# Performance work log

Hardware: AMD Instinct MI355X
Metric: run time of the kernel (lower is better)

## Reference

```python
import jax, jax.numpy as jnp
import numpy as np

B, W, F, H = 2048, 128, 8, 256
LN_EPS = 1e-5


def _gru_cell(h, xt, Wih, Whh, bih, bhh):
    # PyTorch GRU cell. Wih: [3H, Fin], Whh: [3H, H]
    gi = xt @ Wih.T + bih            # [B, 3H]
    gh = h @ Whh.T + bhh             # [B, 3H]
    ir, iz, inn = jnp.split(gi, 3, axis=-1)
    hr, hz, hn = jnp.split(gh, 3, axis=-1)
    r = jax.nn.sigmoid(ir + hr)
    z = jax.nn.sigmoid(iz + hz)
    n = jnp.tanh(inn + r * hn)
    return (1.0 - z) * n + z * h


def setup_inputs() -> dict:
    key = jax.random.key(0)
    ks = jax.random.split(key, 12)
    s = 1.0 / np.sqrt(H)   # torch GRU init: U(-1/sqrt(H), 1/sqrt(H))
    sp = 1.0 / np.sqrt(2 * H)  # torch Linear init fan_in = 2H
    u = lambda k, shp, sc: jax.random.uniform(k, shp, jnp.float32, -sc, sc)
    return {
        "x": jax.random.normal(ks[0], (B, W, F), jnp.float32),
        "Wih_f": u(ks[1], (3 * H, F), s), "Whh_f": u(ks[2], (3 * H, H), s),
        "bih_f": u(ks[3], (3 * H,), s), "bhh_f": u(ks[4], (3 * H,), s),
        "Wih_b": u(ks[5], (3 * H, F), s), "Whh_b": u(ks[6], (3 * H, H), s),
        "bih_b": u(ks[7], (3 * H,), s), "bhh_b": u(ks[8], (3 * H,), s),
        "Wp": u(ks[9], (H, 2 * H), sp), "bp": u(ks[10], (H,), sp),
        "gamma": jnp.ones((H,), jnp.float32), "beta": jnp.zeros((H,), jnp.float32),
    }


def reference(x, Wih_f, Whh_f, bih_f, bhh_f, Wih_b, Whh_b, bih_b, bhh_b, Wp, bp, gamma, beta):
    b = x.shape[0]
    h0 = jnp.zeros((b, H), x.dtype)
    xs = jnp.swapaxes(x, 0, 1)  # [W, B, F]
    # Forward direction: only the final hidden state is used (out[:, -1, :H]).
    h_fwd, _ = jax.lax.scan(
        lambda h, xt: (_gru_cell(h, xt, Wih_f, Whh_f, bih_f, bhh_f), None), h0, xs)
    # Backward direction output at the LAST time index is its FIRST step
    # (reversed scan starting from h0 on x[:, -1]).
    h_bwd = _gru_cell(h0, x[:, -1, :], Wih_b, Whh_b, bih_b, bhh_b)
    last = jnp.concatenate([h_fwd, h_bwd], axis=-1)  # [B, 2H]
    y = jax.nn.gelu(last @ Wp.T + bp, approximate=False)
    mu = jnp.mean(y, axis=-1, keepdims=True)
    var = jnp.var(y, axis=-1, keepdims=True)
    yn = (y - mu) * jax.lax.rsqrt(var + LN_EPS)
    return yn * gamma + beta  # dropout is identity in eval mode
```

## Files before the change

### kernel.cpp

```cpp
#include <hip/hip_runtime.h>
#include <hip/hip_bf16.h>

#define BDIM 2048
#define WDIM 128
#define FDIM 8
#define HDIM 256

typedef __bf16 b8 __attribute__((ext_vector_type(8)));
typedef __bf16 b4 __attribute__((ext_vector_type(4)));
typedef float f32x4 __attribute__((ext_vector_type(4)));
typedef long l64;

#define L2E  1.44269504088896f
#define L2E2 2.88539008177793f

#define OFF_RZ8 0
#define OFF_NB  131072
#define OFF_WI8 262144
#define OFF_WIN 278528
#define OFF_WP  294912
#define OFF_XB  557056

#define MFMA(a,b,c)  __builtin_amdgcn_mfma_f32_16x16x32_bf16((a),(b),(c),0,0,0)
#define MFMA8(a,b,c) __builtin_amdgcn_mfma_f32_16x16x32_fp8_fp8((a),(b),(c),0,0,0)

static __device__ __forceinline__ float sig_(float v) {
    return __builtin_amdgcn_rcpf(1.0f + __expf(-v));
}
static __device__ __forceinline__ float tanh_(float v) {
    return fmaf(-2.0f, __builtin_amdgcn_rcpf(1.0f + __expf(2.0f * v)), 1.0f);
}

static __device__ __forceinline__ l64 pk8(const float* v) {
    int lo = __builtin_amdgcn_cvt_pk_fp8_f32(v[0], v[1], 0, false);
    lo = __builtin_amdgcn_cvt_pk_fp8_f32(v[2], v[3], lo, true);
    int hi = __builtin_amdgcn_cvt_pk_fp8_f32(v[4], v[5], 0, false);
    hi = __builtin_amdgcn_cvt_pk_fp8_f32(v[6], v[7], hi, true);
    return ((l64)(unsigned)hi << 32) | (unsigned)lo;
}
static __device__ __forceinline__ l64 b8_to_f8(b8 v) {
    float f[8];
    #pragma unroll
    for (int e = 0; e < 8; ++e) f[e] = (float)v[e];
    return pk8(f);
}

__global__ void pack_kernel(const float* __restrict__ x,
                            const float* __restrict__ Wih_f,
                            const float* __restrict__ Whh_f,
                            const float* __restrict__ bih_f,
                            const float* __restrict__ bhh_f,
                            const float* __restrict__ Wp,
                            unsigned char* __restrict__ ws)
{
    int idx = blockIdx.x * 256 + threadIdx.x;
    if (idx < 16384) {
        int l = idx & 63, f = idx >> 6;
        int kt = f & 7, nt = (f >> 3) & 1, g = (f >> 4) & 1, w = f >> 5;
        int gch = g * HDIM + 32 * w + 16 * nt + (l & 15);
        int kb = kt * 32 + (l >> 4) * 8;
        float v[8];
        #pragma unroll
        for (int e = 0; e < 8; ++e) v[e] = -L2E * Whh_f[gch * HDIM + kb + e];
        ((l64*)(ws + OFF_RZ8))[idx] = pk8(v);
    } else if (idx < 24576) {
        int j = idx - 16384;
        int l = j & 63, f = j >> 6;
        int kt = f & 7, nt = (f >> 3) & 1, w = f >> 4;
        int gch = 2 * HDIM + 32 * w + 16 * nt + (l & 15);
        int kb = kt * 32 + (l >> 4) * 8;
        b8 v;
        #pragma unroll
        for (int e = 0; e < 8; ++e) v[e] = (__bf16)(L2E2 * Whh_f[gch * HDIM + kb + e]);
        ((b8*)(ws + OFF_NB))[j] = v;
    } else if (idx < 26624) {
        int j = idx - 24576;
        int l = j & 63, f = j >> 6;
        int nt = f & 1, g = (f >> 1) & 1, w = f >> 2;
        int gch = g * HDIM + 32 * w + 16 * nt + (l & 15);
        int lq = l >> 4;
        float v[8];
        #pragma unroll
        for (int e = 0; e < 8; ++e) v[e] = 0.0f;
        if (lq == 0) {
            #pragma unroll
            for (int e = 0; e < 8; ++e) v[e] = -L2E * Wih_f[gch * FDIM + e];
        } else if (lq == 1) {
            v[0] = -L2E * (bih_f[gch] + bhh_f[gch]);
        }
        ((l64*)(ws + OFF_WI8))[j] = pk8(v);
    } else if (idx < 27648) {
        int j = idx - 26624;
        int l = j & 63, f = j >> 6;
        int nt = f & 1, w = f >> 1;
        int gch = 2 * HDIM + 32 * w + 16 * nt + (l & 15);
        int lq = l >> 4;
        b8 v;
        #pragma unroll
        for (int e = 0; e < 8; ++e) v[e] = (__bf16)0.0f;
        if (lq == 0) {
            #pragma unroll
            for (int e = 0; e < 8; ++e) v[e] = (__bf16)(L2E2 * Wih_f[gch * FDIM + e]);
        } else if (lq == 1) {
            v[0] = (__bf16)(L2E2 * bih_f[gch]);
        }
        ((b8*)(ws + OFF_WIN))[j] = v;
    } else if (idx < 44032) {
        int j = idx - 27648;
        int l = j & 63, nk = j >> 6;
        int NT = nk >> 4, kt = nk & 15;
        int col = NT * 16 + (l & 15);
        int kb = kt * 32 + (l >> 4) * 8;
        b8 v;
        #pragma unroll
        for (int e = 0; e < 8; ++e) v[e] = (__bf16)Wp[col * (2 * HDIM) + kb + e];
        ((b8*)(ws + OFF_WP))[j] = v;
    } else if (idx < 44032 + 262144) {
        int j = idx - 44032;
        const float* src = x + j * 8;
        b8 v;
        #pragma unroll
        for (int e = 0; e < 8; ++e) v[e] = (__bf16)src[e];
        ((b8*)(ws + OFF_XB))[j] = v;
    }
}

__global__ __launch_bounds__(512, 2)
void gru_main_kernel(const float* __restrict__ x,
                     const float* __restrict__ bhh_f,
                     const float* __restrict__ Wih_b, const float* __restrict__ bih_b,
                     const float* __restrict__ bhh_b,
                     const float* __restrict__ bp,
                     const float* __restrict__ gamma, const float* __restrict__ beta,
                     const unsigned char* __restrict__ ws,
                     float* __restrict__ out)
{
    __shared__ __align__(16) unsigned char smem[32768];
    __bf16* hbB = (__bf16*)smem;
    unsigned char* hb8 = smem + 16384;
    __bf16 (*lastb)[2 * HDIM] = (__bf16(*)[2 * HDIM])smem;
    float  (*ybuf)[HDIM]      = (float(*)[HDIM])(smem + 16384);

    const int tid = threadIdx.x, lane = tid & 63, w = tid >> 6;
    const int l15 = lane & 15, lq = lane >> 4;
    const int blockRow = blockIdx.x * 16;

    const l64* wsRZ8 = (const l64*)(ws + OFF_RZ8);
    const b8*  wsNB  = (const b8*)(ws + OFF_NB);
    const l64* wsWI8 = (const l64*)(ws + OFF_WI8);
    const b8*  wsWIN = (const b8*)(ws + OFF_WIN);
    const b8*  wsWP  = (const b8*)(ws + OFF_WP);
    const b8*  xB    = (const b8*)(ws + OFF_XB);

    const f32x4 zero4 = {0.f, 0.f, 0.f, 0.f};

    *(f32x4*)(smem + tid * 16) = zero4;
    *(f32x4*)(smem + 8192 + tid * 16) = zero4;
    *(f32x4*)(smem + 16384 + tid * 16) = zero4;

    l64 whr8[2][8], whz8[2][8], wir8[2], wiz8[2];
    b8 wnnB[2][8], winB[2];
    #pragma unroll
    for (int nt = 0; nt < 2; ++nt) {
        #pragma unroll
        for (int kt = 0; kt < 8; ++kt) {
            whr8[nt][kt] = wsRZ8[((w * 4 + 0 + nt) * 8 + kt) * 64 + lane];
            whz8[nt][kt] = wsRZ8[((w * 4 + 2 + nt) * 8 + kt) * 64 + lane];
            wnnB[nt][kt] = wsNB[((w * 2 + nt) * 8 + kt) * 64 + lane];
        }
        wir8[nt] = wsWI8[(w * 4 + 0 + nt) * 64 + lane];
        wiz8[nt] = wsWI8[(w * 4 + 2 + nt) * 64 + lane];
        winB[nt] = wsWIN[(w * 2 + nt) * 64 + lane];
    }
    #pragma unroll
    for (int nt = 0; nt < 2; ++nt) {
        #pragma unroll
        for (int kt = 0; kt < 8; ++kt) {
            asm volatile("" : "+v"(whr8[nt][kt]));
            asm volatile("" : "+v"(whz8[nt][kt]));
            asm volatile("" : "+a"(wnnB[nt][kt]));
        }
        asm volatile("" : "+v"(wir8[nt]));
        asm volatile("" : "+v"(wiz8[nt]));
        asm volatile("" : "+v"(winB[nt]));
    }

    float4 t0v = *(const float4*)&bhh_f[2 * HDIM + 32 * w + 0  + 4 * lq];
    float4 t1v = *(const float4*)&bhh_f[2 * HDIM + 32 * w + 16 + 4 * lq];
    f32x4 bnv0, bnv1;
    bnv0[0] = L2E2 * t0v.x; bnv0[1] = L2E2 * t0v.y; bnv0[2] = L2E2 * t0v.z; bnv0[3] = L2E2 * t0v.w;
    bnv1[0] = L2E2 * t1v.x; bnv1[1] = L2E2 * t1v.y; bnv1[2] = L2E2 * t1v.z; bnv1[3] = L2E2 * t1v.w;

    b8 xc;
    #pragma unroll
    for (int e = 0; e < 8; ++e) xc[e] = (__bf16)0.0f;
    if (lq == 1) xc[0] = (__bf16)1.0f;

    f32x4 h0 = zero4, h1 = zero4;

    const int kswz = (8 * lq) ^ ((l15 & 7) << 3);
    const int wswz = (l15 & 7) << 3;
    const b8* xRow = xB + (blockRow + l15) * WDIM;

    b8 xf = xc;
    if (lane < 16) xf = xRow[0];

    __syncthreads();

    int cur = 0;
    for (int t = 0; t < WDIM; ++t) {
        b8 xn = xc;
        if (lane < 16) xn = xRow[(t + 1) & 127];

        l64 xf8 = b8_to_f8(xf);

        f32x4 aR0 = MFMA8(wir8[0], xf8, zero4);
        f32x4 aR1 = MFMA8(wir8[1], xf8, zero4);
        f32x4 aZ0 = MFMA8(wiz8[0], xf8, zero4);
        f32x4 aZ1 = MFMA8(wiz8[1], xf8, zero4);
        f32x4 aNX0 = MFMA(winB[0], xf, zero4);
        f32x4 aNX1 = MFMA(winB[1], xf, zero4);
        f32x4 aNH0 = bnv0, aNH1 = bnv1;

        const __bf16* hcB = hbB + cur * 4096 + l15 * 256;
        const unsigned char* hc8 = hb8 + cur * 4096 + l15 * 256;
        #pragma unroll
        for (int kt = 0; kt < 8; ++kt) {
            b8 hfB  = *(const b8*)(hcB + ((kt << 5) ^ kswz));
            l64 hf8 = *(const l64*)(hc8 + ((kt << 5) ^ kswz));
            aR0  = MFMA8(whr8[0][kt], hf8, aR0);
            aR1  = MFMA8(whr8[1][kt], hf8, aR1);
            aZ0  = MFMA8(whz8[0][kt], hf8, aZ0);
            aZ1  = MFMA8(whz8[1][kt], hf8, aZ1);
            aNH0 = MFMA(wnnB[0][kt], hfB, aNH0);
            aNH1 = MFMA(wnnB[1][kt], hfB, aNH1);
        }

        __bf16* hnB = hbB + (cur ^ 1) * 4096;
        unsigned char* hn8 = hb8 + (cur ^ 1) * 4096 + l15 * 256;
        b4 v0, v1;
        float hv0[4], hv1[4];
        #pragma unroll
        for (int j = 0; j < 4; ++j) {
            float r = __builtin_amdgcn_rcpf(1.0f + __builtin_amdgcn_exp2f(aR0[j]));
            float z = __builtin_amdgcn_rcpf(1.0f + __builtin_amdgcn_exp2f(aZ0[j]));
            float u = fmaf(r, aNH0[j], aNX0[j]);
            float n = fmaf(-2.0f, __builtin_amdgcn_rcpf(1.0f + __builtin_amdgcn_exp2f(u)), 1.0f);
            float hv = n + z * (h0[j] - n);
            h0[j] = hv; v0[j] = (__bf16)hv; hv0[j] = hv;

            r = __builtin_amdgcn_rcpf(1.0f + __builtin_amdgcn_exp2f(aR1[j]));
            z = __builtin_amdgcn_rcpf(1.0f + __builtin_amdgcn_exp2f(aZ1[j]));
            u = fmaf(r, aNH1[j], aNX1[j]);
            n = fmaf(-2.0f, __builtin_amdgcn_rcpf(1.0f + __builtin_amdgcn_exp2f(u)), 1.0f);
            hv = n + z * (h1[j] - n);
            h1[j] = hv; v1[j] = (__bf16)hv; hv1[j] = hv;
        }
        *(b4*)(hnB + l15 * 256 + ((32 * w + 0  + 4 * lq) ^ wswz)) = v0;
        *(b4*)(hnB + l15 * 256 + ((32 * w + 16 + 4 * lq) ^ wswz)) = v1;
        int p0 = __builtin_amdgcn_cvt_pk_fp8_f32(hv0[0], hv0[1], 0, false);
        p0 = __builtin_amdgcn_cvt_pk_fp8_f32(hv0[2], hv0[3], p0, true);
        int p1 = __builtin_amdgcn_cvt_pk_fp8_f32(hv1[0], hv1[1], 0, false);
        p1 = __builtin_amdgcn_cvt_pk_fp8_f32(hv1[2], hv1[3], p1, true);
        *(int*)(hn8 + ((32 * w + 0  + 4 * lq) ^ wswz)) = p0;
        *(int*)(hn8 + ((32 * w + 16 + 4 * lq) ^ wswz)) = p1;

        xf = xn;
        cur ^= 1;
        __syncthreads();
    }

    {
        b4 v0, v1;
        #pragma unroll
        for (int j = 0; j < 4; ++j) { v0[j] = (__bf16)h0[j]; v1[j] = (__bf16)h1[j]; }
        *(b4*)(&lastb[l15][0] + ((32 * w + 0  + 4 * lq) ^ wswz)) = v0;
        *(b4*)(&lastb[l15][0] + ((32 * w + 16 + 4 * lq) ^ wswz)) = v1;
    }

    {
        const int trow = tid >> 5;
        const int cb = tid & 31;
        const float4* xr = (const float4*)(x + (blockRow + trow) * WDIM * FDIM + 127 * FDIM);
        float4 xv0 = xr[0], xv1 = xr[1];
        const float4* wb = (const float4*)Wih_b;
        #pragma unroll
        for (int jj = 0; jj < 8; ++jj) {
            int ch = cb + 32 * jj;
            float4 a0 = wb[ch * 2],               a1 = wb[ch * 2 + 1];
            float4 b0 = wb[(HDIM + ch) * 2],      b1 = wb[(HDIM + ch) * 2 + 1];
            float4 c0v = wb[(2 * HDIM + ch) * 2], c1 = wb[(2 * HDIM + ch) * 2 + 1];
            float ir = bih_b[ch]
                + xv0.x * a0.x + xv0.y * a0.y + xv0.z * a0.z + xv0.w * a0.w
                + xv1.x * a1.x + xv1.y * a1.y + xv1.z * a1.z + xv1.w * a1.w;
            float iz = bih_b[HDIM + ch]
                + xv0.x * b0.x + xv0.y * b0.y + xv0.z * b0.z + xv0.w * b0.w
                + xv1.x * b1.x + xv1.y * b1.y + xv1.z * b1.z + xv1.w * b1.w;
            float inn = bih_b[2 * HDIM + ch]
                + xv0.x * c0v.x + xv0.y * c0v.y + xv0.z * c0v.z + xv0.w * c0v.w
                + xv1.x * c1.x + xv1.y * c1.y + xv1.z * c1.z + xv1.w * c1.w;
            float r = sig_(ir + bhh_b[ch]);
            float z = sig_(iz + bhh_b[HDIM + ch]);
            float n = tanh_(fmaf(r, bhh_b[2 * HDIM + ch], inn));
            float hbw = (1.0f - z) * n;
            int c2 = HDIM + ch;
            lastb[trow][c2 ^ ((trow & 7) << 3)] = (__bf16)hbw;
        }
    }
    __syncthreads();

    {
        f32x4 pacc[2];
        #pragma unroll
        for (int nt = 0; nt < 2; ++nt) {
            int col = 32 * w + nt * 16 + l15;
            float b = bp[col];
            pacc[nt][0] = b; pacc[nt][1] = b; pacc[nt][2] = b; pacc[nt][3] = b;
        }
        #pragma unroll
        for (int kt = 0; kt < 16; ++kt) {
            int c = (kt * 32 + lq * 8) ^ ((l15 & 7) << 3);
            b8 a = *(const b8*)&lastb[l15][c];
            #pragma unroll
            for (int nt = 0; nt < 2; ++nt)
                pacc[nt] = MFMA(a, wsWP[((2 * w + nt) * 16 + kt) * 64 + lane], pacc[nt]);
        }
        #pragma unroll
        for (int nt = 0; nt < 2; ++nt) {
            int col = 32 * w + nt * 16 + l15;
            #pragma unroll
            for (int j = 0; j < 4; ++j) {
                int row = lq * 4 + j;
                float v = pacc[nt][j];
                ybuf[row][col] = 0.5f * v * (1.0f + erff(v * 0.70710678118f));
            }
        }
    }
    __syncthreads();

    #pragma unroll
    for (int rr = 0; rr < 2; ++rr) {
        int row = 2 * w + rr;
        float v[4];
        float s = 0.0f, sq = 0.0f;
        #pragma unroll
        for (int m = 0; m < 4; ++m) {
            v[m] = ybuf[row][lane + 64 * m];
            s += v[m];
            sq += v[m] * v[m];
        }
        #pragma unroll
        for (int off = 32; off >= 1; off >>= 1) {
            s  += __shfl_xor(s, off, 64);
            sq += __shfl_xor(sq, off, 64);
        }
        float mu = s * (1.0f / 256.0f);
        float var = sq * (1.0f / 256.0f) - mu * mu;
        float rs = rsqrtf(var + 1e-5f);
        float* orow = out + (blockRow + row) * HDIM;
        #pragma unroll
        for (int m = 0; m < 4; ++m) {
            int cc = lane + 64 * m;
            orow[cc] = (v[m] - mu) * rs * gamma[cc] + beta[cc];
        }
    }
}

extern "C" void kernel_launch(void* const* d_in, const int* in_sizes, int n_in,
                              void* d_out, int out_size, void* d_ws, size_t ws_size,
                              hipStream_t stream)
{
    const float* x     = (const float*)d_in[0];
    const float* Wih_f = (const float*)d_in[1];
    const float* Whh_f = (const float*)d_in[2];
    const float* bih_f = (const float*)d_in[3];
    const float* bhh_f = (const float*)d_in[4];
    const float* Wih_b = (const float*)d_in[5];
    const float* bih_b = (const float*)d_in[7];
    const float* bhh_b = (const float*)d_in[8];
    const float* Wp    = (const float*)d_in[9];
    const float* bp    = (const float*)d_in[10];
    const float* gamma = (const float*)d_in[11];
    const float* beta  = (const float*)d_in[12];
    float* out = (float*)d_out;
    unsigned char* ws = (unsigned char*)d_ws;

    const int packItems = 16384 + 8192 + 2048 + 1024 + 16384 + 262144;
    hipLaunchKernelGGL(pack_kernel, dim3((packItems + 255) / 256), dim3(256), 0, stream,
                       x, Wih_f, Whh_f, bih_f, bhh_f, Wp, ws);
    hipLaunchKernelGGL(gru_main_kernel, dim3(BDIM / 16), dim3(512), 0, stream,
                       x, bhh_f, Wih_b, bih_b, bhh_b, bp, gamma, beta, ws, out);
}
```

Measured before the change: 217.0 us.

## Pre-pack x to fp8 and widen fp8 hidden-state LDS reads to 16 bytes

The pack kernel now also writes an fp8 copy of x, so the per-step bf16-to-fp8 conversion inside the recurrent loop is removed. The fp8 hidden-state buffer gets a new permuted, swizzled layout: each step does four 16-byte LDS reads that feed the eight K-tiles, instead of eight 8-byte reads. The aim is fewer VALU conversions and LDS instructions on the serial critical path. In exchange the pack kernel does more work, the workspace grows, and a second global load of x is needed each step. Correctness relies on the new write offsets matching the new K ordering that the weight packing expects.

```diff
diff --git a/kernel.cpp b/kernel.cpp
--- a/kernel.cpp
+++ b/kernel.cpp
@@ -10,6 +10,7 @@
 typedef __bf16 b4 __attribute__((ext_vector_type(4)));
 typedef float f32x4 __attribute__((ext_vector_type(4)));
 typedef long l64;
+typedef l64 l64x2 __attribute__((ext_vector_type(2)));
 
 #define L2E  1.44269504088896f
 #define L2E2 2.88539008177793f
@@ -20,6 +21,7 @@
 #define OFF_WIN 278528
 #define OFF_WP  294912
 #define OFF_XB  557056
+#define OFF_X8  4751360
 
 #define MFMA(a,b,c)  __builtin_amdgcn_mfma_f32_16x16x32_bf16((a),(b),(c),0,0,0)
 #define MFMA8(a,b,c) __builtin_amdgcn_mfma_f32_16x16x32_fp8_fp8((a),(b),(c),0,0,0)
@@ -37,12 +39,6 @@
     int hi = __builtin_amdgcn_cvt_pk_fp8_f32(v[4], v[5], 0, false);
     hi = __builtin_amdgcn_cvt_pk_fp8_f32(v[6], v[7], hi, true);
     return ((l64)(unsigned)hi << 32) | (unsigned)lo;
-}
-static __device__ __forceinline__ l64 b8_to_f8(b8 v) {
-    float f[8];
-    #pragma unroll
-    for (int e = 0; e < 8; ++e) f[e] = (float)v[e];
-    return pk8(f);
 }
 
 __global__ void pack_kernel(const float* __restrict__ x,
@@ -122,6 +118,13 @@
         #pragma unroll
         for (int e = 0; e < 8; ++e) v[e] = (__bf16)src[e];
         ((b8*)(ws + OFF_XB))[j] = v;
+    } else if (idx < 306176 + 262144) {
+        int j = idx - 306176;
+        const float* src = x + j * 8;
+        float v[8];
+        #pragma unroll
+        for (int e = 0; e < 8; ++e) v[e] = src[e];
+        ((l64*)(ws + OFF_X8))[j] = pk8(v);
     }
 }
 
@@ -151,6 +154,7 @@
     const b8*  wsWIN = (const b8*)(ws + OFF_WIN);
     const b8*  wsWP  = (const b8*)(ws + OFF_WP);
     const b8*  xB    = (const b8*)(ws + OFF_XB);
+    const l64* x8    = (const l64*)(ws + OFF_X8);
 
     const f32x4 zero4 = {0.f, 0.f, 0.f, 0.f};
 
@@ -195,24 +199,29 @@
     #pragma unroll
     for (int e = 0; e < 8; ++e) xc[e] = (__bf16)0.0f;
     if (lq == 1) xc[0] = (__bf16)1.0f;
+    const l64 xc8 = (lq == 1) ? (l64)0x38 : (l64)0;
 
     f32x4 h0 = zero4, h1 = zero4;
 
-    const int kswz = (8 * lq) ^ ((l15 & 7) << 3);
-    const int wswz = (l15 & 7) << 3;
-    const b8* xRow = xB + (blockRow + l15) * WDIM;
-
-    b8 xf = xc;
-    if (lane < 16) xf = xRow[0];
+    const int kswz  = (8 * lq) ^ ((l15 & 7) << 3);
+    const int wswz  = (l15 & 7) << 3;
+    const int swz16 = (l15 & 7) << 4;
+    const int wbase = ((w & 3) * 64) + ((w >> 2) * 8) + 4 * (lq & 1);
+    const int wof0  = (wbase + ((lq >> 1) + 0) * 16) ^ swz16;
+    const int wof1  = (wbase + ((lq >> 1) + 2) * 16) ^ swz16;
+
+    const b8*  xRow  = xB + (blockRow + l15) * WDIM;
+    const l64* x8Row = x8 + (blockRow + l15) * WDIM;
+
+    b8 xf = xc; l64 xf8 = xc8;
+    if (lane < 16) { xf = xRow[0]; xf8 = x8Row[0]; }
 
     __syncthreads();
 
     int cur = 0;
     for (int t = 0; t < WDIM; ++t) {
-        b8 xn = xc;
-        if (lane < 16) xn = xRow[(t + 1) & 127];
-
-        l64 xf8 = b8_to_f8(xf);
+        b8 xn = xc; l64 xn8 = xc8;
+        if (lane < 16) { xn = xRow[(t + 1) & 127]; xn8 = x8Row[(t + 1) & 127]; }
 
         f32x4 aR0 = MFMA8(wir8[0], xf8, zero4);
         f32x4 aR1 = MFMA8(wir8[1], xf8, zero4);
@@ -224,10 +233,16 @@
 
         const __bf16* hcB = hbB + cur * 4096 + l15 * 256;
         const unsigned char* hc8 = hb8 + cur * 4096 + l15 * 256;
+
+        l64x2 h8p[4];
+        #pragma unroll
+        for (int p = 0; p < 4; ++p)
+            h8p[p] = *(const l64x2*)(hc8 + ((p * 64 + lq * 16) ^ swz16));
+
         #pragma unroll
         for (int kt = 0; kt < 8; ++kt) {
             b8 hfB  = *(const b8*)(hcB + ((kt << 5) ^ kswz));
-            l64 hf8 = *(const l64*)(hc8 + ((kt << 5) ^ kswz));
+            l64 hf8 = (kt < 4) ? h8p[kt][0] : h8p[kt - 4][1];
             aR0  = MFMA8(whr8[0][kt], hf8, aR0);
             aR1  = MFMA8(whr8[1][kt], hf8, aR1);
             aZ0  = MFMA8(whz8[0][kt], hf8, aZ0);
@@ -262,10 +277,10 @@
         p0 = __builtin_amdgcn_cvt_pk_fp8_f32(hv0[2], hv0[3], p0, true);
         int p1 = __builtin_amdgcn_cvt_pk_fp8_f32(hv1[0], hv1[1], 0, false);
         p1 = __builtin_amdgcn_cvt_pk_fp8_f32(hv1[2], hv1[3], p1, true);
-        *(int*)(hn8 + ((32 * w + 0  + 4 * lq) ^ wswz)) = p0;
-        *(int*)(hn8 + ((32 * w + 16 + 4 * lq) ^ wswz)) = p1;
-
-        xf = xn;
+        *(int*)(hn8 + wof0) = p0;
+        *(int*)(hn8 + wof1) = p1;
+
+        xf = xn; xf8 = xn8;
         cur ^= 1;
         __syncthreads();
     }
@@ -385,7 +400,7 @@
     float* out = (float*)d_out;
     unsigned char* ws = (unsigned char*)d_ws;
 
-    const int packItems = 16384 + 8192 + 2048 + 1024 + 16384 + 262144;
+    const int packItems = 306176 + 262144;
     hipLaunchKernelGGL(pack_kernel, dim3((packItems + 255) / 256), dim3(256), 0, stream,
                        x, Wih_f, Whh_f, bih_f, bhh_f, Wp, ws);
     hipLaunchKernelGGL(gru_main_kernel, dim3(BDIM / 16), dim3(512), 0, stream,
```

Result: no change. 218.1 us (+0.5%).
